# Performance work log

Hardware: AMD Instinct MI355X
Metric: run time of the kernel (lower is better)

## Reference

```python
import jax, jax.numpy as jnp
import numpy as np

S, B, D, H, HD = 2048, 4, 1280, 16, 80  # seq, batch, d_model, heads, head_dim
NSEG = 8


def setup_inputs() -> dict:
    key = jax.random.key(0)
    k0, k1, k2 = jax.random.split(key, 3)
    x = jax.random.normal(k0, (S, B, D), dtype=jnp.float32)
    Wqkv = jax.random.normal(k1, (D, 3 * D), dtype=jnp.float32) * 0.02
    bqkv = jnp.zeros((3 * D,), dtype=jnp.float32)
    Wproj = jax.random.normal(k2, (D, 4 * D), dtype=jnp.float32) * 0.02
    bproj = jnp.zeros((4 * D,), dtype=jnp.float32)
    # 8 equal windows of 256 tokens: [0, 256, 512, ..., 2048]
    cu_seqlens = (jnp.arange(NSEG + 1, dtype=jnp.int32) * (S // NSEG))
    return {"x": x, "Wqkv": Wqkv, "bqkv": bqkv, "Wproj": Wproj,
            "bproj": bproj, "cu_seqlens": cu_seqlens}


def reference(x, Wqkv, bqkv, Wproj, bproj, cu_seqlens):
    s, b, d = x.shape
    qkv = x @ Wqkv + bqkv                     # [s, b, 3d]
    q, k, v = jnp.split(qkv, 3, axis=2)       # each [s, b, d]
    def to_bhsd(t):
        return t.reshape(s, b, H, HD).transpose(1, 2, 0, 3)  # [b, h, s, hd]
    q, k, v = to_bhsd(q), to_bhsd(k), to_bhsd(v)
    # Block-diagonal mask: token t belongs to window searchsorted(cu[1:], t, right)
    pos = jnp.arange(s)
    seg = jnp.searchsorted(cu_seqlens[1:], pos, side='right')  # [s]
    bias = jnp.where(seg[:, None] == seg[None, :], 0.0,
                     jnp.finfo(x.dtype).min)                   # [s, s]
    scale = 1.0 / jnp.sqrt(jnp.asarray(HD, dtype=x.dtype))
    scores = jnp.einsum('bhsd,bhtd->bhst', q, k) * scale + bias
    attn = jax.nn.softmax(scores, axis=-1)
    out = jnp.einsum('bhst,bhtd->bhsd', attn, v)               # [b, h, s, hd]
    context = out.transpose(2, 0, 1, 3).reshape(s, b, H * HD)  # [s, b, d]
    return context @ Wproj + bproj                             # [s, b, 4d]
```

## Files before the change

### kernel.cpp

```cpp
#include <hip/hip_runtime.h>

typedef _Float16 f16;
typedef _Float16 f16x8 __attribute__((ext_vector_type(8)));
typedef _Float16 f16x4 __attribute__((ext_vector_type(4)));
typedef float    f32x4 __attribute__((ext_vector_type(4)));
typedef unsigned int u32t;

#define AS1 __attribute__((address_space(1)))
#define AS3 __attribute__((address_space(3)))

static __device__ __forceinline__ void gload_lds16(const void* g, void* l) {
  __builtin_amdgcn_global_load_lds((const AS1 u32t*)g, (AS3 u32t*)l, 16, 0, 0);
}

static __device__ __forceinline__ f16x8 zero8() {
  f16x8 z;
#pragma unroll
  for (int j = 0; j < 8; ++j) z[j] = (f16)0;
  return z;
}

__global__ void k_cvt_x(const float* __restrict__ in, f16* __restrict__ out, int n4) {
  int stride = gridDim.x * blockDim.x;
  for (int i = blockIdx.x * blockDim.x + threadIdx.x; i < n4; i += stride) {
    float4 v = ((const float4*)in)[i];
    f16x4 o;
    o[0] = (f16)v.x; o[1] = (f16)v.y; o[2] = (f16)v.z; o[3] = (f16)v.w;
    ((f16x4*)out)[i] = o;
  }
}

__global__ void k_cvt_w_t(const float* __restrict__ W, f16* __restrict__ Wt, int N) {
  __shared__ float T[32][33];
  int bk = blockIdx.x % 40;
  int bn = blockIdx.x / 40;
  int k0 = bk * 32, n0 = bn * 32;
  int r = threadIdx.x >> 5;
  int c = threadIdx.x & 31;
#pragma unroll
  for (int i = 0; i < 4; ++i)
    T[r + i * 8][c] = W[(size_t)(k0 + r + i * 8) * N + n0 + c];
  __syncthreads();
#pragma unroll
  for (int i = 0; i < 4; ++i)
    Wt[(size_t)(n0 + r + i * 8) * 1280 + k0 + c] = (f16)T[c][r + i * 8];
}


template<int NCOLS, bool F16OUT>
__global__ __launch_bounds__(512, 1)
void gemm_nt(const f16* __restrict__ A, const f16* __restrict__ Bt,
             const float* __restrict__ bias, void* __restrict__ Cout)
{
  __shared__ __align__(16) char lds[131072];
  const int tid = threadIdx.x;
  const int wave = tid >> 6, lane = tid & 63;
  const int rl = lane & 15, g = lane >> 4;
  const int wm = wave >> 2, wn = wave & 3;

  constexpr int NBN = NCOLS / 256;
  constexpr int NWG = 32 * NBN;
  const int bid = blockIdx.x;
  const int wgid = (bid & 7) * (NWG / 8) + (bid >> 3);
  const int bm = wgid / NBN, bn = wgid % NBN;
  const long row0 = (long)bm * 256, col0 = (long)bn * 256;

  const int subA = wave * 8 + (lane >> 3);
  const int cpA  = (((lane & 7) ^ (subA & 7)) << 4);
  const char* gAt = (const char*)A + (row0 + subA) * 2560 + cpA;
  const int subB = (wave & 3) * 8 + (lane >> 3);
  const int cpB  = (((lane & 7) ^ (subB & 7)) << 4);
  const char* gBt = (const char*)Bt + (col0 + (wave >> 2) * 64 + subB) * 2560 + cpB;
  char* const dA = lds + wave * 1024;
  char* const dB = lds + 65536 + wave * 1024;

  auto STA = [&](int mh, int buf, int kb) {
#pragma unroll
    for (int l = 0; l < 2; ++l)
      gload_lds16(gAt + mh * (64 * 2560) + l * (128 * 2560) + kb,
                  dA + buf * 32768 + mh * 16384 + l * 8192);
  };
  auto STB = [&](int nh, int buf, int kb) {
#pragma unroll
    for (int l = 0; l < 2; ++l)
      gload_lds16(gBt + nh * (32 * 2560) + l * (128 * 2560) + kb,
                  dB + buf * 32768 + nh * 16384 + l * 8192);
  };

  const int swz0 = ((0 + g) ^ (rl & 7)) << 4;
  const int swz1 = ((4 + g) ^ (rl & 7)) << 4;
  const int aro = wm * 8192 + rl * 128;
  const int bro = 65536 + wn * 4096 + rl * 128;

  auto LDA = [&](f16x8 (&af)[8], int buf, int mh) {
#pragma unroll
    for (int m = 0; m < 4; ++m) {
      const char* p = lds + buf * 32768 + mh * 16384 + aro + m * 2048;
      af[m * 2 + 0] = *(const f16x8*)(p + swz0);
      af[m * 2 + 1] = *(const f16x8*)(p + swz1);
    }
  };
  auto LDB = [&](f16x8 (&bf)[4], int buf, int nh) {
#pragma unroll
    for (int n = 0; n < 2; ++n) {
      const char* p = lds + buf * 32768 + nh * 16384 + bro + n * 2048;
      bf[n * 2 + 0] = *(const f16x8*)(p + swz0);
      bf[n * 2 + 1] = *(const f16x8*)(p + swz1);
    }
  };

  f32x4 acc[8][4];
#pragma unroll
  for (int m = 0; m < 8; ++m)
#pragma unroll
    for (int n = 0; n < 4; ++n) acc[m][n] = (f32x4){0.f, 0.f, 0.f, 0.f};

  auto MM = [&](int mh, int nh, const f16x8 (&af)[8], const f16x8 (&bf)[4]) {
    __builtin_amdgcn_s_setprio(1);
#pragma unroll
    for (int m = 0; m < 4; ++m)
#pragma unroll
      for (int n = 0; n < 2; ++n)
#pragma unroll
        for (int kk = 0; kk < 2; ++kk)
          acc[mh * 4 + m][nh * 2 + n] = __builtin_amdgcn_mfma_f32_16x16x32_f16(
              af[m * 2 + kk], bf[n * 2 + kk], acc[mh * 4 + m][nh * 2 + n], 0, 0, 0);
    __builtin_amdgcn_s_setprio(0);
  };

#define BAR()   do { __builtin_amdgcn_s_barrier(); asm volatile("" ::: "memory"); } while (0)
#define WLGKM() asm volatile("s_waitcnt lgkmcnt(0)" ::: "memory")
#define WVM(N)  asm volatile("s_waitcnt vmcnt(" #N ")" ::: "memory")

  auto TILE = [&](int buf, int kbB1, int kbN, int mode) {
    f16x8 af[8], bf0[4], bf1[4];
    LDA(af, buf, 0); LDB(bf0, buf, 0);
    if (mode <= 1) STB(1, buf ^ 1, kbB1);
    BAR(); WLGKM(); MM(0, 0, af, bf0); BAR();
    LDB(bf1, buf, 1);
    if (mode == 0) STA(0, buf, kbN);
    BAR(); WLGKM(); MM(0, 1, af, bf1); BAR();
    LDA(af, buf, 1);
    if (mode == 0) STB(0, buf, kbN);
    BAR(); WLGKM(); MM(1, 1, af, bf1); BAR();
    if (mode == 0) STA(1, buf, kbN);
    if (mode == 0) { WVM(6); } else if (mode == 1) { WVM(0); }
    BAR(); MM(1, 0, af, bf0);
    if (mode != 2) BAR();
  };

  STA(0, 0, 0); STB(0, 0, 0); STA(1, 0, 0); STB(1, 0, 0);
  STA(0, 1, 128); STB(0, 1, 128); STA(1, 1, 128);
  WVM(6); BAR();

#pragma unroll 1
  for (int it = 0; it < 9; ++it) {
    const int kb = it * 256;
    TILE(0, kb + 128, kb + 256, 0);
    TILE(1, kb + 256, kb + 384, 0);
  }
  TILE(0, 2432, 0, 1);
  TILE(1, 0, 0, 2);

#undef BAR
#undef WLGKM
#undef WVM

#pragma unroll
  for (int m = 0; m < 8; ++m) {
#pragma unroll
    for (int n = 0; n < 4; ++n) {
      long c = col0 + wn * 64 + n * 16 + rl;
      float bv = bias[c];
#pragma unroll
      for (int r = 0; r < 4; ++r) {
        long rr = row0 + wm * 128 + m * 16 + g * 4 + r;
        float v = acc[m][n][r] + bv;
        if (F16OUT) ((f16*)Cout)[rr * NCOLS + c] = (f16)v;
        else        ((float*)Cout)[rr * NCOLS + c] = v;
      }
    }
  }
}

__global__ void k_vt(const f16* __restrict__ qkv, f16* __restrict__ vt) {
  __shared__ __align__(16) f16 T[128 * 136];
  int bid = blockIdx.x;
  int sc16 = bid & 15, bh = bid >> 4;
  int b = bh >> 4, h = bh & 15;
  int s0 = sc16 * 128;
  int t = threadIdx.x;
#pragma unroll
  for (int i = 0; i < 5; ++i) {
    int cid = i * 256 + t;
    int s = cid / 10, c = cid % 10;
    const f16* g = qkv + (size_t)((s0 + s) * 4 + b) * 3840 + 2560 + h * 80 + c * 8;
    f16x8 v = *(const f16x8*)g;
    int phys = c ^ ((s >> 3) & 7);
    *(f16x8*)(T + s * 136 + phys * 8) = v;
  }
  __syncthreads();
#pragma unroll
  for (int i = 0; i < 5; ++i) {
    int oid = i * 256 + t;
    int sc8 = oid & 15, hd = oid >> 4;
    f16x8 o;
#pragma unroll
    for (int j = 0; j < 8; ++j) {
      int row = sc8 * 8 + j;
      int phys = (hd >> 3) ^ (sc8 & 7);
      o[j] = T[row * 136 + phys * 8 + (hd & 7)];
    }
    *(f16x8*)(vt + (size_t)(bh * 80 + hd) * 2048 + s0 + sc8 * 8) = o;
  }
}

__global__ __launch_bounds__(512, 2)
void k_attn(const f16* __restrict__ qkv, const f16* __restrict__ vt,
            f16* __restrict__ ctx)
{
  __shared__ __align__(16) f16 sK[256 * 104];
  __shared__ __align__(16) f16 sV[80 * 264];
  __shared__ __align__(16) f16 sP[256 * 72];

  const int bid = blockIdx.x;
  const int seg = bid & 7, h = (bid >> 3) & 15, b = bid >> 7;
  const int t = threadIdx.x;
  const int wave = t >> 6, lane = t & 63;
  const int s_key0 = seg * 256;

#pragma unroll
  for (int i = 0; i < 5; ++i) {
    int cid = i * 512 + t;
    int key = cid / 10, c = cid % 10;
    const f16* g = qkv + (size_t)((s_key0 + key) * 4 + b) * 3840 + 1280 + h * 80 + c * 8;
    *(f16x8*)(sK + key * 104 + c * 8) = *(const f16x8*)g;
  }
  {
    int key = t >> 1, c = t & 1;
    *(f16x8*)(sK + key * 104 + 80 + c * 8) = zero8();
  }
#pragma unroll
  for (int i = 0; i < 5; ++i) {
    int cid = i * 512 + t;
    int hd = cid >> 5, c = cid & 31;
    const f16* g = vt + (size_t)((b * 16 + h) * 80 + hd) * 2048 + s_key0 + c * 8;
    *(f16x8*)(sV + hd * 264 + c * 8) = *(const f16x8*)g;
  }

  const int q0 = s_key0 + wave * 32;
  const int rl = lane & 15, g = lane >> 4;
  f16x8 qfl[3], qfh[3];
  {
    const f16* gl = qkv + (size_t)((q0 + rl) * 4 + b) * 3840 + h * 80;
    const f16* gh = qkv + (size_t)((q0 + 16 + rl) * 4 + b) * 3840 + h * 80;
    qfl[0] = *(const f16x8*)(gl + g * 8);
    qfh[0] = *(const f16x8*)(gh + g * 8);
    qfl[1] = *(const f16x8*)(gl + 32 + g * 8);
    qfh[1] = *(const f16x8*)(gh + 32 + g * 8);
    if (g < 2) { qfl[2] = *(const f16x8*)(gl + 64 + g * 8); qfh[2] = *(const f16x8*)(gh + 64 + g * 8); }
    else       { qfl[2] = zero8(); qfh[2] = zero8(); }
  }
  __syncthreads();

  f32x4 scl[16], sch[16];
#pragma unroll
  for (int nt = 0; nt < 16; ++nt) { scl[nt] = (f32x4){0.f,0.f,0.f,0.f}; sch[nt] = (f32x4){0.f,0.f,0.f,0.f}; }
#pragma unroll
  for (int nt = 0; nt < 16; ++nt) {
#pragma unroll
    for (int kk = 0; kk < 3; ++kk) {
      f16x8 bf = *(const f16x8*)(sK + (nt * 16 + rl) * 104 + kk * 32 + g * 8);
      scl[nt] = __builtin_amdgcn_mfma_f32_16x16x32_f16(qfl[kk], bf, scl[nt], 0, 0, 0);
      sch[nt] = __builtin_amdgcn_mfma_f32_16x16x32_f16(qfh[kk], bf, sch[nt], 0, 0, 0);
    }
  }

  const float scale = 0.11180339887498949f;
  float invl[4], invh[4];
#pragma unroll
  for (int r = 0; r < 4; ++r) {
    float ml = -1e30f, mh = -1e30f;
#pragma unroll
    for (int nt = 0; nt < 16; ++nt) { ml = fmaxf(ml, scl[nt][r]); mh = fmaxf(mh, sch[nt][r]); }
#pragma unroll
    for (int off = 8; off >= 1; off >>= 1) { ml = fmaxf(ml, __shfl_xor(ml, off)); mh = fmaxf(mh, __shfl_xor(mh, off)); }
    ml *= scale; mh *= scale;
    float suml = 0.f, sumh = 0.f;
#pragma unroll
    for (int nt = 0; nt < 16; ++nt) {
      float pl = __expf(scl[nt][r] * scale - ml);
      float ph = __expf(sch[nt][r] * scale - mh);
      scl[nt][r] = pl; sch[nt][r] = ph;
      suml += pl; sumh += ph;
    }
#pragma unroll
    for (int off = 8; off >= 1; off >>= 1) { suml += __shfl_xor(suml, off); sumh += __shfl_xor(sumh, off); }
    invl[r] = 1.0f / suml; invh[r] = 1.0f / sumh;
  }

  f32x4 ol[5], oh[5];
#pragma unroll
  for (int nt = 0; nt < 5; ++nt) { ol[nt] = (f32x4){0.f,0.f,0.f,0.f}; oh[nt] = (f32x4){0.f,0.f,0.f,0.f}; }
  const int prow0 = wave * 32;
  for (int ch = 0; ch < 4; ++ch) {
#pragma unroll
    for (int f = 0; f < 4; ++f) {
      int nt = ch * 4 + f;
#pragma unroll
      for (int r = 0; r < 4; ++r) {
        sP[(prow0 + g * 4 + r) * 72 + f * 16 + rl]      = (f16)scl[nt][r];
        sP[(prow0 + 16 + g * 4 + r) * 72 + f * 16 + rl] = (f16)sch[nt][r];
      }
    }
#pragma unroll
    for (int kk = 0; kk < 2; ++kk) {
      f16x8 pal = *(const f16x8*)(sP + (prow0 + rl) * 72 + kk * 32 + g * 8);
      f16x8 pah = *(const f16x8*)(sP + (prow0 + 16 + rl) * 72 + kk * 32 + g * 8);
#pragma unroll
      for (int nt = 0; nt < 5; ++nt) {
        f16x8 vb = *(const f16x8*)(sV + (nt * 16 + rl) * 264 + ch * 64 + kk * 32 + g * 8);
        ol[nt] = __builtin_amdgcn_mfma_f32_16x16x32_f16(pal, vb, ol[nt], 0, 0, 0);
        oh[nt] = __builtin_amdgcn_mfma_f32_16x16x32_f16(pah, vb, oh[nt], 0, 0, 0);
      }
    }
  }

#pragma unroll
  for (int nt = 0; nt < 5; ++nt) {
    int hd = nt * 16 + rl;
#pragma unroll
    for (int r = 0; r < 4; ++r) {
      long qrl = q0 + g * 4 + r;
      ctx[(qrl * 4 + b) * 1280 + h * 80 + hd] = (f16)(ol[nt][r] * invl[r]);
      long qrh = q0 + 16 + g * 4 + r;
      ctx[(qrh * 4 + b) * 1280 + h * 80 + hd] = (f16)(oh[nt][r] * invh[r]);
    }
  }
}

extern "C" void kernel_launch(void* const* d_in, const int* in_sizes, int n_in,
                              void* d_out, int out_size, void* d_ws, size_t ws_size,
                              hipStream_t stream)
{
  const float* x     = (const float*)d_in[0];
  const float* Wqkv  = (const float*)d_in[1];
  const float* bqkv  = (const float*)d_in[2];
  const float* Wproj = (const float*)d_in[3];
  const float* bproj = (const float*)d_in[4];

  char* ws = (char*)d_ws;
  f16* X16   = (f16*)(ws);
  f16* WQT   = (f16*)(ws + 20971520);
  f16* WPT   = (f16*)(ws + 30801920);
  f16* QKV16 = (f16*)(ws + 43909120);
  f16* VT    = (f16*)(ws + 106823680);
  f16* CTX16 = X16;

  k_cvt_x<<<4096, 256, 0, stream>>>(x, X16, 8192 * 1280 / 4);
  k_cvt_w_t<<<40 * 120, 256, 0, stream>>>(Wqkv, WQT, 3840);
  k_cvt_w_t<<<40 * 160, 256, 0, stream>>>(Wproj, WPT, 5120);
  gemm_nt<3840, true ><<<480, 512, 0, stream>>>(X16, WQT, bqkv, QKV16);
  k_vt<<<1024, 256, 0, stream>>>(QKV16, VT);
  k_attn<<<512, 512, 0, stream>>>(QKV16, VT, CTX16);
  gemm_nt<5120, false><<<640, 512, 0, stream>>>(CTX16, WPT, bproj, d_out);
}
```

Before: 271.8 us.

## Use 128x128-tile GEMM with LDS-staged coalesced stores for output projection

Adds a new 128x128 tile GEMM kernel with 256 threads and two blocks per CU, and uses it for the fp32 output projection instead of the 256x256 kernel. It launches 2560 blocks rather than 640, which spreads work across CUs more evenly. The epilogue stages results in swizzled LDS so each row is written with coalesced 16-byte fp32 stores. The cost is a single-buffered K loop with no prefetch and lower operand reuse per tile.

```diff
diff --git a/kernel.cpp b/kernel.cpp
--- a/kernel.cpp
+++ b/kernel.cpp
@@ -46,11 +46,10 @@
     Wt[(size_t)(n0 + r + i * 8) * 1280 + k0 + c] = (f16)T[c][r + i * 8];
 }
 
-
 template<int NCOLS, bool F16OUT>
 __global__ __launch_bounds__(512, 1)
-void gemm_nt(const f16* __restrict__ A, const f16* __restrict__ Bt,
-             const float* __restrict__ bias, void* __restrict__ Cout)
+void gemm_nt256(const f16* __restrict__ A, const f16* __restrict__ Bt,
+                const float* __restrict__ bias, void* __restrict__ Cout)
 {
   __shared__ __align__(16) char lds[131072];
   const int tid = threadIdx.x;
@@ -183,6 +182,105 @@
   }
 }
 
+template<int NCOLS>
+__global__ __launch_bounds__(256, 2)
+void gemm_nt128(const f16* __restrict__ A, const f16* __restrict__ Bt,
+                const float* __restrict__ bias, float* __restrict__ Cout)
+{
+  __shared__ __align__(16) char lds[32768];
+  f16* const sA = (f16*)lds;
+  f16* const sB = (f16*)(lds + 16384);
+  const int tid = threadIdx.x;
+  const int wave = tid >> 6, lane = tid & 63;
+  constexpr int NBN = NCOLS / 128;
+  const int bm = blockIdx.x / NBN, bn = blockIdx.x % NBN;
+  const long row0 = (long)bm * 128, col0 = (long)bn * 128;
+
+  f32x4 acc[4][4];
+#pragma unroll
+  for (int i = 0; i < 4; ++i)
+#pragma unroll
+    for (int j = 0; j < 4; ++j) acc[i][j] = (f32x4){0.f, 0.f, 0.f, 0.f};
+
+  const int wr = (wave >> 1) * 64, wc = (wave & 1) * 64;
+
+  int segr[4], segoff[4];
+#pragma unroll
+  for (int i = 0; i < 4; ++i) {
+    int o = (wave * 4 + i) * 1024 + lane * 16;
+    int r = o >> 7, cb = o & 127;
+    segr[i] = r;
+    segoff[i] = cb ^ ((r & 7) << 4);
+  }
+
+  const char* Ab = (const char*)A;
+  const char* Bb = (const char*)Bt;
+
+  for (int kt = 0; kt < 20; ++kt) {
+    __syncthreads();
+#pragma unroll
+    for (int i = 0; i < 4; ++i) {
+      const char* ga = Ab + ((row0 + segr[i]) * 1280 + kt * 64) * 2 + segoff[i];
+      gload_lds16(ga, (char*)sA + (wave * 4 + i) * 1024);
+      const char* gb = Bb + ((col0 + segr[i]) * 1280 + kt * 64) * 2 + segoff[i];
+      gload_lds16(gb, (char*)sB + (wave * 4 + i) * 1024);
+    }
+    __syncthreads();
+
+#pragma unroll
+    for (int kk = 0; kk < 2; ++kk) {
+      const int rl = lane & 15, g = lane >> 4, x7 = lane & 7;
+      const int ph = (kk * 4 + g) ^ x7;
+      f16x8 af[4], bf[4];
+#pragma unroll
+      for (int mt = 0; mt < 4; ++mt)
+        af[mt] = *(const f16x8*)(sA + (wr + mt * 16 + rl) * 64 + ph * 8);
+#pragma unroll
+      for (int nt = 0; nt < 4; ++nt)
+        bf[nt] = *(const f16x8*)(sB + (wc + nt * 16 + rl) * 64 + ph * 8);
+#pragma unroll
+      for (int mt = 0; mt < 4; ++mt)
+#pragma unroll
+        for (int nt = 0; nt < 4; ++nt)
+          acc[mt][nt] = __builtin_amdgcn_mfma_f32_16x16x32_f16(af[mt], bf[nt], acc[mt][nt], 0, 0, 0);
+    }
+  }
+
+  {
+    float* bb = (float*)lds;
+    const int rl = lane & 15, g = lane >> 4;
+    const int wm = wave >> 1;
+    const int lrow = tid >> 2, q = tid & 3;
+#pragma unroll
+    for (int p = 0; p < 2; ++p) {
+      __syncthreads();
+#pragma unroll
+      for (int mt2 = 0; mt2 < 2; ++mt2) {
+        int mt = p * 2 + mt2;
+#pragma unroll
+        for (int nt = 0; nt < 4; ++nt) {
+          int col = wc + nt * 16 + rl;
+          float bv = bias[col0 + col];
+#pragma unroll
+          for (int r = 0; r < 4; ++r) {
+            int clrow = wm * 32 + mt2 * 16 + g * 4 + r;
+            bb[clrow * 128 + (col ^ ((clrow & 7) << 2))] = acc[mt][nt][r] + bv;
+          }
+        }
+      }
+      __syncthreads();
+      long grow = row0 + (lrow >> 5) * 64 + p * 32 + (lrow & 31);
+      float* gout = Cout + grow * NCOLS + col0;
+#pragma unroll
+      for (int j = 0; j < 8; ++j) {
+        int col = j * 16 + q * 4;
+        f32x4 v = *(const f32x4*)(bb + lrow * 128 + (col ^ ((lrow & 7) << 2)));
+        *(f32x4*)(gout + col) = v;
+      }
+    }
+  }
+}
+
 __global__ void k_vt(const f16* __restrict__ qkv, f16* __restrict__ vt) {
   __shared__ __align__(16) f16 T[128 * 136];
   int bid = blockIdx.x;
@@ -360,8 +458,8 @@
   k_cvt_x<<<4096, 256, 0, stream>>>(x, X16, 8192 * 1280 / 4);
   k_cvt_w_t<<<40 * 120, 256, 0, stream>>>(Wqkv, WQT, 3840);
   k_cvt_w_t<<<40 * 160, 256, 0, stream>>>(Wproj, WPT, 5120);
-  gemm_nt<3840, true ><<<480, 512, 0, stream>>>(X16, WQT, bqkv, QKV16);
+  gemm_nt256<3840, true><<<480, 512, 0, stream>>>(X16, WQT, bqkv, QKV16);
   k_vt<<<1024, 256, 0, stream>>>(QKV16, VT);
   k_attn<<<512, 512, 0, stream>>>(QKV16, VT, CTX16);
-  gemm_nt<5120, false><<<640, 512, 0, stream>>>(CTX16, WPT, bproj, d_out);
-}
+  gemm_nt128<5120><<<64 * 40, 256, 0, stream>>>(CTX16, WPT, bproj, (float*)d_out);
+}
```

Result: faster. 258.5 us (-4.9%).
